# Kernel optimization log

Hardware: AMD Instinct MI355X
Metric: run time of the kernel (lower is better)

## Reference

```python
import jax, jax.numpy as jnp
import numpy as np

B, S, D, H = 64, 1024, 128, 256  # batch, seq, input_dim, hidden_dim


def _glorot(key, shape):
    fan_in, fan_out = shape[0], shape[-1]
    lim = np.sqrt(6.0 / (fan_in + fan_out)).astype(np.float32)
    return jax.random.uniform(key, shape, jnp.float32, -lim, lim)


def setup_inputs() -> dict:
    key = jax.random.key(0)
    ks = jax.random.split(key, 13)
    inp = {
        "x": jax.random.normal(ks[0], (B, S, D), jnp.float32),
        # forward-direction lite-GRU params
        "Wz_f": _glorot(ks[1], (D, H)), "Uz_f": _glorot(ks[2], (H, H)), "bz_f": jnp.zeros((H,), jnp.float32),
        "Wh_f": _glorot(ks[3], (D, H)), "Uh_f": _glorot(ks[4], (H, H)), "bh_f": jnp.zeros((H,), jnp.float32),
        # backward-direction lite-GRU params
        "Wz_b": _glorot(ks[5], (D, H)), "Uz_b": _glorot(ks[6], (H, H)), "bz_b": jnp.zeros((H,), jnp.float32),
        "Wh_b": _glorot(ks[7], (D, H)), "Uh_b": _glorot(ks[8], (H, H)), "bh_b": jnp.zeros((H,), jnp.float32),
        # attention: Linear(2H,2H) -> Tanh -> Linear(2H,1) -> Softmax(dim=1)
        "W1": _glorot(ks[9], (2 * H, 2 * H)), "b1": jnp.zeros((2 * H,), jnp.float32),
        "w2": _glorot(ks[10], (2 * H, 1)), "b2": jnp.zeros((1,), jnp.float32),
    }
    return inp


def _lite_gru(x, Wz, Uz, bz, Wh, Uh, bh):
    # x: [B,S,D] -> outputs [B,S,H]; lite GRU (no reset gate)
    xz = jnp.einsum('bsd,dh->bsh', x, Wz) + bz  # precompute input projections
    xh = jnp.einsum('bsd,dh->bsh', x, Wh) + bh

    def step(h, inps):
        xz_t, xh_t = inps  # [B,H]
        z = jax.nn.sigmoid(xz_t + h @ Uz)
        hc = jnp.tanh(xh_t + h @ Uh)
        h = z * h + (1.0 - z) * hc
        return h, h

    h0 = jnp.zeros((x.shape[0], Uz.shape[0]), x.dtype)
    _, ys = jax.lax.scan(step, h0, (jnp.swapaxes(xz, 0, 1), jnp.swapaxes(xh, 0, 1)))
    return jnp.swapaxes(ys, 0, 1)  # [B,S,H]


def reference(x, Wz_f, Uz_f, bz_f, Wh_f, Uh_f, bh_f,
              Wz_b, Uz_b, bz_b, Wh_b, Uh_b, bh_b, W1, b1, w2, b2):
    out_f = _lite_gru(x, Wz_f, Uz_f, bz_f, Wh_f, Uh_f, bh_f)
    out_b = _lite_gru(x[:, ::-1, :], Wz_b, Uz_b, bz_b, Wh_b, Uh_b, bh_b)[:, ::-1, :]
    out = jnp.concatenate([out_f, out_b], axis=-1)  # [B,S,2H]
    # additive attention: Linear -> tanh -> Linear -> softmax over time
    scores = jnp.tanh(out @ W1 + b1) @ w2 + b2       # [B,S,1]
    attn = jax.nn.softmax(scores, axis=1)
    context = jnp.sum(attn * out, axis=1)            # [B,2H]
    return context
```

## Files before the change

### kernel.cpp

```cpp
#include <hip/hip_runtime.h>
#include <cstdint>
#include <cstddef>

typedef _Float16 f16;
typedef _Float16 f16x8 __attribute__((ext_vector_type(8)));
typedef _Float16 f16x4 __attribute__((ext_vector_type(4)));
typedef _Float16 f16x2 __attribute__((ext_vector_type(2)));
typedef float f32x4 __attribute__((ext_vector_type(4)));

#define MFMA16(a, b, c) __builtin_amdgcn_mfma_f32_16x16x32_f16((a), (b), (c), 0, 0, 0)


static constexpr size_t UT_OFF  = 0;
static constexpr size_t WT_OFF  = 524288;
static constexpr size_t W1T_OFF = 786432;
static constexpr size_t XP_OFF  = 1310720;
static constexpr size_t OUT_OFF = XP_OFF + 134217728;
static constexpr size_t SC_OFF  = OUT_OFF + 67108864;
static constexpr size_t AT_OFF  = SC_OFF + 262144;
static constexpr size_t PART_OFF= AT_OFF + 262144;

__global__ void k0_prep(const float* __restrict__ Uzf, const float* __restrict__ Uhf,
                        const float* __restrict__ Uzb, const float* __restrict__ Uhb,
                        const float* __restrict__ Wzf, const float* __restrict__ Whf,
                        const float* __restrict__ Wzb, const float* __restrict__ Whb,
                        const float* __restrict__ W1,
                        f16* __restrict__ Ut, f16* __restrict__ Wt, f16* __restrict__ W1t)
{
    int tid = blockIdx.x * blockDim.x + threadIdx.x;
    int nthr = gridDim.x * blockDim.x;
    for (int i = tid; i < 4 * 256 * 256; i += nthr) {
        int u = i >> 16, cc = (i >> 8) & 255, k = i & 255;
        const float* U = (u == 0) ? Uzf : (u == 1) ? Uhf : (u == 2) ? Uzb : Uhb;
        Ut[i] = (f16)U[k * 256 + cc];
    }
    for (int i = tid; i < 2 * 512 * 128; i += nthr) {
        int dir = i >> 16, cc2 = (i >> 7) & 511, k = i & 127;
        const float* W = dir ? ((cc2 & 256) ? Whb : Wzb) : ((cc2 & 256) ? Whf : Wzf);
        Wt[i] = (f16)W[k * 256 + (cc2 & 255)];
    }
    for (int i = tid; i < 512 * 512; i += nthr) {
        int n = i >> 9, k = i & 511;
        W1t[i] = (f16)W1[k * 512 + n];
    }
}

__launch_bounds__(256, 2)
__global__ void k1_xproj(const float* __restrict__ x, const f16* __restrict__ Wt,
                         const float* __restrict__ bzf, const float* __restrict__ bhf,
                         const float* __restrict__ bzb, const float* __restrict__ bhb,
                         f16* __restrict__ xp2)
{
    int bid = blockIdx.x;
    int s = bid & 1023, g = (bid >> 10) & 3, dir = bid >> 12;
    int s_src = dir ? (1023 - s) : s;
    int tid = threadIdx.x, w = tid >> 6, lane = tid & 63, q = lane >> 4, l16 = lane & 15;

    f16x8 bf[4];
    const float* xr = x + ((size_t)(g * 16 + l16) * 1024 + s_src) * 128;
#pragma unroll
    for (int kt = 0; kt < 4; ++kt) {
        int k0 = kt * 32 + q * 8;
        f32x4 a = *(const f32x4*)(xr + k0);
        f32x4 c = *(const f32x4*)(xr + k0 + 4);
        f16x8 v;
#pragma unroll
        for (int j = 0; j < 4; ++j) { v[j] = (f16)a[j]; v[4 + j] = (f16)c[j]; }
        bf[kt] = v;
    }
    const f16* wt = Wt + (size_t)dir * 512 * 128;
    f16x8 af[8][4];
#pragma unroll
    for (int mt = 0; mt < 8; ++mt) {
        int cc2 = w * 128 + mt * 16 + l16;
#pragma unroll
        for (int kt = 0; kt < 4; ++kt)
            af[mt][kt] = *(const f16x8*)(wt + cc2 * 128 + kt * 32 + q * 8);
    }
    f32x4 acc[8];
#pragma unroll
    for (int mt = 0; mt < 8; ++mt) acc[mt] = (f32x4){0.f, 0.f, 0.f, 0.f};
#pragma unroll
    for (int kt = 0; kt < 4; ++kt)
#pragma unroll
        for (int mt = 0; mt < 8; ++mt)
            acc[mt] = MFMA16(af[mt][kt], bf[kt], acc[mt]);

    f16* dst = xp2 + (size_t)((dir * 4 + g) * 1024 + s) * 8192;
#pragma unroll
    for (int mt = 0; mt < 8; ++mt) {
        int ccg = w * 128 + mt * 16 + q * 4;
        int gate = ccg >> 8, c = ccg & 255;
        const float* bias = gate ? (dir ? bhb : bhf) : (dir ? bzb : bzf);
        f32x4 bi = *(const f32x4*)(bias + c);
        f16x4 o;
#pragma unroll
        for (int r = 0; r < 4; ++r) o[r] = (f16)(acc[mt][r] + bi[r]);
        int flat = ((gate * 2 + ((c >> 4) & 1)) * 8 + (c >> 5)) * 256 + (q * 16 + l16) * 4;
        *(f16x4*)(dst + flat) = o;
    }
}

__launch_bounds__(512, 2)
__global__ void k2_gru(const f16* __restrict__ Ut, const f16* __restrict__ xp2,
                       f16* __restrict__ out16)
{
    int bid = blockIdx.x;
    int dir = bid >> 2, g = bid & 3;
    int tid = threadIdx.x, w = tid >> 6, lane = tid & 63, q = lane >> 4, l16 = lane & 15;
    __shared__ f16 h16[2][16][264];
    __shared__ f16 ob[8][16][264];

    for (int i = tid; i < 2 * 16 * 264; i += 512) (&h16[0][0][0])[i] = (f16)0.f;

    f16x8 uf[4][8];
#pragma unroll
    for (int t = 0; t < 4; ++t) {
        int gate = t >> 1;
        int cc = w * 32 + (t & 1) * 16 + l16;
        const f16* up = Ut + ((size_t)(dir * 2 + gate) * 256 + cc) * 256;
#pragma unroll
        for (int kt = 0; kt < 8; ++kt)
            uf[t][kt] = *(const volatile f16x8*)(up + kt * 32 + q * 8);
    }

    const f16* xb = xp2 + (size_t)(dir * 4 + g) * 1024 * 8192;
    int offs[4];
#pragma unroll
    for (int t = 0; t < 4; ++t) {
        int gate = t >> 1, p = t & 1;
        offs[t] = ((gate * 2 + p) * 8 + w) * 256 + lane * 4;
    }
    f16x4 cx[4];
#pragma unroll
    for (int t = 0; t < 4; ++t) cx[t] = *(const f16x4*)(xb + offs[t]);
    f32x4 hold[2];
    hold[0] = (f32x4){0.f, 0.f, 0.f, 0.f};
    hold[1] = (f32x4){0.f, 0.f, 0.f, 0.f};

    __syncthreads();

    for (int so = 0; so < 1024; so += 8) {
#pragma unroll
        for (int si = 0; si < 8; ++si) {
            int s = so + si;
            int cur = s & 1, nxt = cur ^ 1;
            const f16* px = xb + (size_t)((s + 1 < 1024) ? s + 1 : s) * 8192;
            f16x4 nx[4];
#pragma unroll
            for (int t = 0; t < 4; ++t) nx[t] = *(const f16x4*)(px + offs[t]);

            f16x8 bf[8];
#pragma unroll
            for (int kt = 0; kt < 8; ++kt)
                bf[kt] = *(const f16x8*)&h16[cur][l16][kt * 32 + q * 8];

            f32x4 acc[4];
#pragma unroll
            for (int t = 0; t < 4; ++t)
#pragma unroll
                for (int r = 0; r < 4; ++r) acc[t][r] = (float)cx[t][r];

#pragma unroll
            for (int kt = 0; kt < 8; ++kt)
#pragma unroll
                for (int t = 0; t < 4; ++t)
                    acc[t] = MFMA16(uf[t][kt], bf[kt], acc[t]);

#pragma unroll
            for (int p = 0; p < 2; ++p) {
                f32x4 hn; f16x4 hh;
#pragma unroll
                for (int r = 0; r < 4; ++r) {
                    float az = acc[p][r];
                    float ah = acc[2 + p][r];
                    float E1 = __expf(-az);
                    float E2 = __expf(-2.f * ah);
                    float h0 = hold[p][r];
                    float num = __builtin_fmaf(h0, E2, h0) + __builtin_fmaf(-E1, E2, E1);
                    float den = (1.f + E1) * (1.f + E2);
                    float hv = num * __builtin_amdgcn_rcpf(den);
                    hn[r] = hv; hh[r] = (f16)hv;
                }
                hold[p] = hn;
                int ccg = w * 32 + p * 16 + q * 4;
                *(f16x4*)&h16[nxt][l16][ccg] = hh;
                *(f16x4*)&ob[si][l16][ccg] = hh;
            }

#pragma unroll
            for (int t = 0; t < 4; ++t) cx[t] = nx[t];
            __syncthreads();
        }
#pragma unroll
        for (int i = 0; i < 8; ++i) {
            int chunk = i * 512 + tid;
            int st = chunk >> 9, rem = chunk & 511;
            int bb2 = rem >> 5, c16 = (rem & 31) * 8;
            int sidx = so + st;
            int s_out = dir ? (1023 - sidx) : sidx;
            f16x8 v = *(const f16x8*)&ob[st][bb2][c16];
            *(f16x8*)(out16 + ((size_t)(g * 16 + bb2) * 1024 + s_out) * 512 + dir * 256 + c16) = v;
        }
        __syncthreads();
    }
}

__launch_bounds__(256, 2)
__global__ void k3_scores(const f16* __restrict__ out16, const f16* __restrict__ W1t,
                          const float* __restrict__ b1, const float* __restrict__ w2,
                          const float* __restrict__ b2, float* __restrict__ scores)
{
    int bid = blockIdx.x;
    int b = bid >> 4, sc = bid & 15, s0 = sc * 64;
    int tid = threadIdx.x, w = tid >> 6, lane = tid & 63, q = lane >> 4, l16 = lane & 15;
    f32x4 acc[4][8];
#pragma unroll
    for (int mt = 0; mt < 4; ++mt)
#pragma unroll
        for (int nt = 0; nt < 8; ++nt) acc[mt][nt] = (f32x4){0.f, 0.f, 0.f, 0.f};

    for (int kt = 0; kt < 16; ++kt) {
        f16x8 af[4];
#pragma unroll
        for (int mt = 0; mt < 4; ++mt) {
            size_t row = (size_t)b * 1024 + s0 + mt * 16 + l16;
            af[mt] = *(const f16x8*)(out16 + row * 512 + kt * 32 + q * 8);
        }
        f16x8 bfg[8];
#pragma unroll
        for (int nt = 0; nt < 8; ++nt) {
            int ncol = w * 128 + nt * 16 + l16;
            bfg[nt] = *(const f16x8*)(W1t + (size_t)ncol * 512 + kt * 32 + q * 8);
        }
#pragma unroll
        for (int mt = 0; mt < 4; ++mt)
#pragma unroll
            for (int nt = 0; nt < 8; ++nt)
                acc[mt][nt] = MFMA16(af[mt], bfg[nt], acc[mt][nt]);
    }
    float b1v[8], w2v[8];
#pragma unroll
    for (int nt = 0; nt < 8; ++nt) {
        int ncol = w * 128 + nt * 16 + l16;
        b1v[nt] = b1[ncol];
        w2v[nt] = w2[ncol];
    }
    __shared__ float spart[4][64];
    float rs[4][4];
#pragma unroll
    for (int mt = 0; mt < 4; ++mt)
#pragma unroll
        for (int r = 0; r < 4; ++r) {
            float ssum = 0.f;
#pragma unroll
            for (int nt = 0; nt < 8; ++nt) {
                float xv = acc[mt][nt][r] + b1v[nt];
                float t = 1.f - 2.f / (1.f + __expf(2.f * xv));
                ssum += t * w2v[nt];
            }
            rs[mt][r] = ssum;
        }
#pragma unroll
    for (int off = 1; off < 16; off <<= 1)
#pragma unroll
        for (int mt = 0; mt < 4; ++mt)
#pragma unroll
            for (int r = 0; r < 4; ++r)
                rs[mt][r] += __shfl_xor(rs[mt][r], off, 64);
    if (l16 == 0) {
#pragma unroll
        for (int mt = 0; mt < 4; ++mt)
#pragma unroll
            for (int r = 0; r < 4; ++r)
                spart[w][mt * 16 + q * 4 + r] = rs[mt][r];
    }
    __syncthreads();
    if (tid < 64) {
        float v = spart[0][tid] + spart[1][tid] + spart[2][tid] + spart[3][tid] + b2[0];
        scores[b * 1024 + s0 + tid] = v;
    }
}

__global__ void k3_softmax(const float* __restrict__ scores, float* __restrict__ attn)
{
    int b = blockIdx.x, tid = threadIdx.x;
    __shared__ float red[4];
    f32x4 v = *(const f32x4*)(scores + b * 1024 + tid * 4);
    float m = fmaxf(fmaxf(v[0], v[1]), fmaxf(v[2], v[3]));
#pragma unroll
    for (int off = 1; off < 64; off <<= 1) m = fmaxf(m, __shfl_xor(m, off, 64));
    if ((tid & 63) == 0) red[tid >> 6] = m;
    __syncthreads();
    m = fmaxf(fmaxf(red[0], red[1]), fmaxf(red[2], red[3]));
    __syncthreads();
    float e0 = __expf(v[0] - m), e1 = __expf(v[1] - m), e2 = __expf(v[2] - m), e3 = __expf(v[3] - m);
    float ssum = e0 + e1 + e2 + e3;
#pragma unroll
    for (int off = 1; off < 64; off <<= 1) ssum += __shfl_xor(ssum, off, 64);
    if ((tid & 63) == 0) red[tid >> 6] = ssum;
    __syncthreads();
    float inv = 1.f / (red[0] + red[1] + red[2] + red[3]);
    f32x4 o = {e0 * inv, e1 * inv, e2 * inv, e3 * inv};
    *(f32x4*)(attn + b * 1024 + tid * 4) = o;
}

__global__ void k3_wsum(const f16* __restrict__ out16, const float* __restrict__ attn,
                        float* __restrict__ part)
{
    int bid = blockIdx.x;
    int b = bid >> 3, ch = bid & 7;
    int tid = threadIdx.x;
    const f16* op = out16 + ((size_t)b * 1024 + ch * 128) * 512 + tid * 2;
    const float* ap = attn + b * 1024 + ch * 128;
    float a0 = 0.f, a1 = 0.f;
#pragma unroll 4
    for (int i = 0; i < 128; ++i) {
        float aw = ap[i];
        f16x2 xv = *(const f16x2*)(op + (size_t)i * 512);
        a0 += aw * (float)xv[0];
        a1 += aw * (float)xv[1];
    }
    part[(size_t)(b * 8 + ch) * 512 + tid * 2] = a0;
    part[(size_t)(b * 8 + ch) * 512 + tid * 2 + 1] = a1;
}

__global__ void k3_final(const float* __restrict__ part, float* __restrict__ outp)
{
    int b = blockIdx.x, tid = threadIdx.x;
#pragma unroll
    for (int j = 0; j < 2; ++j) {
        int cc = tid * 2 + j;
        float ssum = 0.f;
#pragma unroll
        for (int ch = 0; ch < 8; ++ch) ssum += part[(size_t)(b * 8 + ch) * 512 + cc];
        outp[b * 512 + cc] = ssum;
    }
}

extern "C" void kernel_launch(void* const* d_in, const int* in_sizes, int n_in,
                              void* d_out, int out_size, void* d_ws, size_t ws_size,
                              hipStream_t stream)
{
    const float* x   = (const float*)d_in[0];
    const float* Wzf = (const float*)d_in[1];
    const float* Uzf = (const float*)d_in[2];
    const float* bzf = (const float*)d_in[3];
    const float* Whf = (const float*)d_in[4];
    const float* Uhf = (const float*)d_in[5];
    const float* bhf = (const float*)d_in[6];
    const float* Wzb = (const float*)d_in[7];
    const float* Uzb = (const float*)d_in[8];
    const float* bzb = (const float*)d_in[9];
    const float* Whb = (const float*)d_in[10];
    const float* Uhb = (const float*)d_in[11];
    const float* bhb = (const float*)d_in[12];
    const float* W1  = (const float*)d_in[13];
    const float* b1  = (const float*)d_in[14];
    const float* w2  = (const float*)d_in[15];
    const float* b2  = (const float*)d_in[16];
    float* outp = (float*)d_out;

    char* ws = (char*)d_ws;
    f16* Ut    = (f16*)(ws + UT_OFF);
    f16* Wt    = (f16*)(ws + WT_OFF);
    f16* W1t   = (f16*)(ws + W1T_OFF);
    f16* xp2   = (f16*)(ws + XP_OFF);
    f16* o16   = (f16*)(ws + OUT_OFF);
    float* sc  = (float*)(ws + SC_OFF);
    float* at  = (float*)(ws + AT_OFF);
    float* pt  = (float*)(ws + PART_OFF);

    hipLaunchKernelGGL(k0_prep, dim3(256), dim3(256), 0, stream,
                       Uzf, Uhf, Uzb, Uhb, Wzf, Whf, Wzb, Whb, W1, Ut, Wt, W1t);
    hipLaunchKernelGGL(k1_xproj, dim3(8192), dim3(256), 0, stream,
                       x, Wt, bzf, bhf, bzb, bhb, xp2);
    hipLaunchKernelGGL(k2_gru, dim3(8), dim3(512), 0, stream, Ut, xp2, o16);
    hipLaunchKernelGGL(k3_scores, dim3(1024), dim3(256), 0, stream, o16, W1t, b1, w2, b2, sc);
    hipLaunchKernelGGL(k3_softmax, dim3(64), dim3(256), 0, stream, sc, at);
    hipLaunchKernelGGL(k3_wsum, dim3(512), dim3(256), 0, stream, o16, at, pt);
    hipLaunchKernelGGL(k3_final, dim3(64), dim3(256), 0, stream, pt, outp);
}
```

Baseline: 1.439 ms.

## Replace per-step block barrier with split-group LDS flag sync in GRU recurrence

The GRU recurrence kernel no longer uses __syncthreads every timestep. It splits the 8 waves into two groups of 4, each bumping its own LDS counter. Each wave waits on its own group's flag before consuming the first half of the K dimension of h, and on the other group's flag before the second half, with K order swizzled per group so own-group data is consumed first. Gate scaling by log2(e) is folded into the U/W weights and biases so exp2 can be used directly. Outputs are written straight to global memory instead of staged through LDS. The tradeoff is the risk of spin-wait overhead, memory-ordering subtleties with the relaxed atomics, and less coalesced output stores.

```diff
diff --git a/kernel.cpp b/kernel.cpp
--- a/kernel.cpp
+++ b/kernel.cpp
@@ -20,6 +20,17 @@
 static constexpr size_t AT_OFF  = SC_OFF + 262144;
 static constexpr size_t PART_OFF= AT_OFF + 262144;
 
+#define SCALE_Z 1.4426950408889634f
+#define SCALE_H 2.8853900817779268f
+
+__device__ __forceinline__ float fexp2(float x) {
+#if __has_builtin(__builtin_amdgcn_exp2f)
+    return __builtin_amdgcn_exp2f(x);
+#else
+    return __expf(x * 0.6931471805599453f);
+#endif
+}
+
 __global__ void k0_prep(const float* __restrict__ Uzf, const float* __restrict__ Uhf,
                         const float* __restrict__ Uzb, const float* __restrict__ Uhb,
                         const float* __restrict__ Wzf, const float* __restrict__ Whf,
@@ -32,7 +43,8 @@
     for (int i = tid; i < 4 * 256 * 256; i += nthr) {
         int u = i >> 16, cc = (i >> 8) & 255, k = i & 255;
         const float* U = (u == 0) ? Uzf : (u == 1) ? Uhf : (u == 2) ? Uzb : Uhb;
-        Ut[i] = (f16)U[k * 256 + cc];
+        float sg = (u & 1) ? SCALE_H : SCALE_Z;
+        Ut[i] = (f16)(U[k * 256 + cc] * sg);
     }
     for (int i = tid; i < 2 * 512 * 128; i += nthr) {
         int dir = i >> 16, cc2 = (i >> 7) & 511, k = i & 127;
@@ -92,13 +104,20 @@
         int ccg = w * 128 + mt * 16 + q * 4;
         int gate = ccg >> 8, c = ccg & 255;
         const float* bias = gate ? (dir ? bhb : bhf) : (dir ? bzb : bzf);
+        float sg = gate ? SCALE_H : SCALE_Z;
         f32x4 bi = *(const f32x4*)(bias + c);
         f16x4 o;
 #pragma unroll
-        for (int r = 0; r < 4; ++r) o[r] = (f16)(acc[mt][r] + bi[r]);
+        for (int r = 0; r < 4; ++r) o[r] = (f16)((acc[mt][r] + bi[r]) * sg);
         int flat = ((gate * 2 + ((c >> 4) & 1)) * 8 + (c >> 5)) * 256 + (q * 16 + l16) * 4;
         *(f16x4*)(dst + flat) = o;
     }
+}
+
+__device__ __forceinline__ void flag_wait(const int* f, int tgt) {
+    const volatile int* vf = (const volatile int*)f;
+    while (*vf < tgt) __builtin_amdgcn_s_sleep(1);
+    asm volatile("s_waitcnt lgkmcnt(0)" ::: "memory");
 }
 
 __launch_bounds__(512, 2)
@@ -108,10 +127,14 @@
     int bid = blockIdx.x;
     int dir = bid >> 2, g = bid & 3;
     int tid = threadIdx.x, w = tid >> 6, lane = tid & 63, q = lane >> 4, l16 = lane & 15;
+    int grp = w >> 2;
+    int kxor = grp << 2;
+
     __shared__ f16 h16[2][16][264];
-    __shared__ f16 ob[8][16][264];
+    __shared__ int flags[2];
 
     for (int i = tid; i < 2 * 16 * 264; i += 512) (&h16[0][0][0])[i] = (f16)0.f;
+    if (tid == 0) { flags[0] = 0; flags[1] = 0; }
 
     f16x8 uf[4][8];
 #pragma unroll
@@ -120,8 +143,8 @@
         int cc = w * 32 + (t & 1) * 16 + l16;
         const f16* up = Ut + ((size_t)(dir * 2 + gate) * 256 + cc) * 256;
 #pragma unroll
-        for (int kt = 0; kt < 8; ++kt)
-            uf[t][kt] = *(const volatile f16x8*)(up + kt * 32 + q * 8);
+        for (int j = 0; j < 8; ++j)
+            uf[t][j] = *(const volatile f16x8*)(up + (j ^ kxor) * 32 + q * 8);
     }
 
     const f16* xb = xp2 + (size_t)(dir * 4 + g) * 1024 * 8192;
@@ -138,71 +161,81 @@
     hold[0] = (f32x4){0.f, 0.f, 0.f, 0.f};
     hold[1] = (f32x4){0.f, 0.f, 0.f, 0.f};
 
+    f16* op = out16 + ((size_t)(g * 16 + l16) * 1024 + (dir ? 1023 : 0)) * 512
+            + dir * 256 + w * 32 + q * 4;
+    ptrdiff_t sstep = dir ? -512 : 512;
+
+    int* fOwn = &flags[grp];
+    int* fOth = &flags[grp ^ 1];
+
     __syncthreads();
-
-    for (int so = 0; so < 1024; so += 8) {
-#pragma unroll
-        for (int si = 0; si < 8; ++si) {
-            int s = so + si;
-            int cur = s & 1, nxt = cur ^ 1;
-            const f16* px = xb + (size_t)((s + 1 < 1024) ? s + 1 : s) * 8192;
-            f16x4 nx[4];
-#pragma unroll
-            for (int t = 0; t < 4; ++t) nx[t] = *(const f16x4*)(px + offs[t]);
-
-            f16x8 bf[8];
-#pragma unroll
-            for (int kt = 0; kt < 8; ++kt)
-                bf[kt] = *(const f16x8*)&h16[cur][l16][kt * 32 + q * 8];
-
-            f32x4 acc[4];
+    if (grp) __builtin_amdgcn_s_sleep(6);
+
+#pragma unroll 2
+    for (int s = 0; s < 1024; ++s) {
+        int cur = s & 1, nxt = cur ^ 1;
+
+        const f16* px = xb + (size_t)((s + 1 < 1024) ? s + 1 : s) * 8192;
+        f16x4 nx[4];
+#pragma unroll
+        for (int t = 0; t < 4; ++t) nx[t] = *(const f16x4*)(px + offs[t]);
+
+        f32x4 acc[4];
+#pragma unroll
+        for (int t = 0; t < 4; ++t)
+#pragma unroll
+            for (int r = 0; r < 4; ++r) acc[t][r] = (float)cx[t][r];
+
+        int tgt = 4 * s;
+
+        flag_wait(fOwn, tgt);
+        f16x8 bf[8];
+#pragma unroll
+        for (int j = 0; j < 4; ++j)
+            bf[j] = *(const f16x8*)&h16[cur][l16][(j ^ kxor) * 32 + q * 8];
+#pragma unroll
+        for (int j = 0; j < 4; ++j)
 #pragma unroll
             for (int t = 0; t < 4; ++t)
-#pragma unroll
-                for (int r = 0; r < 4; ++r) acc[t][r] = (float)cx[t][r];
-
-#pragma unroll
-            for (int kt = 0; kt < 8; ++kt)
-#pragma unroll
-                for (int t = 0; t < 4; ++t)
-                    acc[t] = MFMA16(uf[t][kt], bf[kt], acc[t]);
-
-#pragma unroll
-            for (int p = 0; p < 2; ++p) {
-                f32x4 hn; f16x4 hh;
-#pragma unroll
-                for (int r = 0; r < 4; ++r) {
-                    float az = acc[p][r];
-                    float ah = acc[2 + p][r];
-                    float E1 = __expf(-az);
-                    float E2 = __expf(-2.f * ah);
-                    float h0 = hold[p][r];
-                    float num = __builtin_fmaf(h0, E2, h0) + __builtin_fmaf(-E1, E2, E1);
-                    float den = (1.f + E1) * (1.f + E2);
-                    float hv = num * __builtin_amdgcn_rcpf(den);
-                    hn[r] = hv; hh[r] = (f16)hv;
-                }
-                hold[p] = hn;
-                int ccg = w * 32 + p * 16 + q * 4;
-                *(f16x4*)&h16[nxt][l16][ccg] = hh;
-                *(f16x4*)&ob[si][l16][ccg] = hh;
+                acc[t] = MFMA16(uf[t][j], bf[j], acc[t]);
+
+        flag_wait(fOth, tgt);
+#pragma unroll
+        for (int j = 4; j < 8; ++j)
+            bf[j] = *(const f16x8*)&h16[cur][l16][(j ^ kxor) * 32 + q * 8];
+#pragma unroll
+        for (int j = 4; j < 8; ++j)
+#pragma unroll
+            for (int t = 0; t < 4; ++t)
+                acc[t] = MFMA16(uf[t][j], bf[j], acc[t]);
+
+#pragma unroll
+        for (int p = 0; p < 2; ++p) {
+            f32x4 hn; f16x4 hh;
+#pragma unroll
+            for (int r = 0; r < 4; ++r) {
+                float az = acc[p][r];
+                float ah = acc[2 + p][r];
+                float E1 = fexp2(-az);
+                float E2 = fexp2(-ah);
+                float h0 = hold[p][r];
+                float num = __builtin_fmaf(h0, E2, h0) + __builtin_fmaf(-E1, E2, E1);
+                float den = (1.f + E1) * (1.f + E2);
+                float hv = num * __builtin_amdgcn_rcpf(den);
+                hn[r] = hv; hh[r] = (f16)hv;
             }
-
-#pragma unroll
-            for (int t = 0; t < 4; ++t) cx[t] = nx[t];
-            __syncthreads();
+            hold[p] = hn;
+            int ccg = w * 32 + p * 16 + q * 4;
+            *(f16x4*)&h16[nxt][l16][ccg] = hh;
+            *(f16x4*)(op + p * 16) = hh;
         }
-#pragma unroll
-        for (int i = 0; i < 8; ++i) {
-            int chunk = i * 512 + tid;
-            int st = chunk >> 9, rem = chunk & 511;
-            int bb2 = rem >> 5, c16 = (rem & 31) * 8;
-            int sidx = so + st;
-            int s_out = dir ? (1023 - sidx) : sidx;
-            f16x8 v = *(const f16x8*)&ob[st][bb2][c16];
-            *(f16x8*)(out16 + ((size_t)(g * 16 + bb2) * 1024 + s_out) * 512 + dir * 256 + c16) = v;
-        }
-        __syncthreads();
+        asm volatile("s_waitcnt lgkmcnt(0)" ::: "memory");
+        if (lane == 0)
+            __hip_atomic_fetch_add(fOwn, 1, __ATOMIC_RELAXED, __HIP_MEMORY_SCOPE_WORKGROUP);
+
+        op += sstep;
+#pragma unroll
+        for (int t = 0; t < 4; ++t) cx[t] = nx[t];
     }
 }
 
```

Result: slower. 1.612 ms (+12.0%).
